# Optimization experiments

Hardware: AMD Instinct MI355X
Metric: run time of the kernel (lower is better)

## Reference

```python
import jax, jax.numpy as jnp
import numpy as np

B, T, V, F = 8, 12, 2048, 16
K_CHEB, C = 3, 64

def setup_inputs() -> dict:
    key = jax.random.key(0)
    k1, k2, k3, k4 = jax.random.split(key, 4)
    x = jax.random.normal(k1, (B, T, V, F), dtype=jnp.float32)
    Att = jax.random.uniform(k2, (B, V, V), dtype=jnp.float32)
    cheb = jax.random.normal(k3, (K_CHEB, V, V), dtype=jnp.float32) / np.sqrt(V)
    theta = jax.random.normal(k4, (K_CHEB, F, C), dtype=jnp.float32) * 0.05
    return {"x": x, "Att": Att, "cheb": cheb, "theta": theta}

def reference(x, Att, cheb, theta):
    # Attention-masked Chebyshev polynomials: S_k[b,u,v] = T_k[u,v] * Att[b,u,v]
    # (dropout from the original training-time call is omitted: eval mode)
    masked = cheb[:, None, :, :] * Att[None, :, :, :]            # (K,B,V,V)
    # rhs[b,v,f] = sum_u S_k[b,u,v] * x[b,t,u,f]  (transpose+batch_dot)
    rhs = jnp.einsum('kbuv,btuf->kbtvf', masked, x)              # (K,B,T,V,F)
    # sum over Chebyshev order k of rhs @ Theta_k, then relu
    out = jnp.einsum('kbtvf,kfc->btvc', rhs, theta)              # (B,T,V,C)
    return jax.nn.relu(out)
```

## Files before the change

### kernel.cpp

```cpp
#include <hip/hip_runtime.h>
#include <hip/hip_bf16.h>
#include <stdint.h>

#define B_  8
#define T_  12
#define V_  2048
#define F_  16
#define K_  3
#define C_  64
#define N_  192

typedef _Float16 f16;
typedef _Float16 half4v __attribute__((ext_vector_type(4)));
typedef _Float16 half8v __attribute__((ext_vector_type(8)));
typedef float    f32x4  __attribute__((ext_vector_type(4)));
typedef float    f32x16 __attribute__((ext_vector_type(16)));
typedef unsigned int u32;

__global__ __launch_bounds__(256) void prep_xt(const float* __restrict__ x,
                                               f16* __restrict__ XT) {
  int bid = blockIdx.x;
  int bt = bid >> 2, uc = bid & 3;
  int b = bt / T_, t = bt % T_;
  __shared__ float tile[64][17];
  int r  = threadIdx.x >> 2, fq = threadIdx.x & 3;
  int f  = threadIdx.x >> 4, uq = threadIdx.x & 15;
  for (int u0 = uc * 512; u0 < uc * 512 + 512; u0 += 64) {
    f32x4 v = *(const f32x4*)(x + ((size_t)(b * T_ + t) * V_ + u0 + r) * F_ + fq * 4);
    tile[r][fq * 4 + 0] = v[0];
    tile[r][fq * 4 + 1] = v[1];
    tile[r][fq * 4 + 2] = v[2];
    tile[r][fq * 4 + 3] = v[3];
    __syncthreads();
    half4v h;
    h[0] = (f16)tile[uq * 4 + 0][f];
    h[1] = (f16)tile[uq * 4 + 1][f];
    h[2] = (f16)tile[uq * 4 + 2][f];
    h[3] = (f16)tile[uq * 4 + 3][f];
    *(half4v*)(XT + (size_t)(b * N_ + t * F_ + f) * V_ + u0 + uq * 4) = h;
    __syncthreads();
  }
}

__global__ __launch_bounds__(256) void prep_chebT(const float* __restrict__ c,
                                                  f16* __restrict__ cT) {
  int bid = blockIdx.x;
  int vt = bid & 31, ut = (bid >> 5) & 31, k = bid >> 10;
  int u0 = ut * 64, v0 = vt * 64;
  __shared__ float tile[64][68];
  int tid = threadIdx.x;
  int lr = tid >> 4, lc = (tid & 15) * 4;
  const float* src = c + ((size_t)k * V_ + u0) * V_ + v0;
#pragma unroll
  for (int i = 0; i < 4; ++i) {
    f32x4 v = *(const f32x4*)(src + (size_t)(lr + 16 * i) * V_ + lc);
    tile[lr + 16 * i][lc + 0] = v[0];
    tile[lr + 16 * i][lc + 1] = v[1];
    tile[lr + 16 * i][lc + 2] = v[2];
    tile[lr + 16 * i][lc + 3] = v[3];
  }
  __syncthreads();
  int vl = tid & 63, uc0 = tid >> 6;
#pragma unroll
  for (int i = 0; i < 2; ++i) {
    int uc = uc0 + 4 * i;
    half8v h;
#pragma unroll
    for (int j = 0; j < 8; ++j) h[j] = (f16)tile[uc * 8 + j][vl];
    int vb = (v0 + vl) >> 5;
    int vi = vl & 31;
    size_t ut_idx = (size_t)(u0 >> 3) + uc;
    size_t off = ((((size_t)k * 64 + vb) * 256 + ut_idx) * 32 + vi) * 8;
    *(half8v*)(cT + off) = h;
  }
}

#define MFMA_H(a, b, c) __builtin_amdgcn_mfma_f32_32x32x16_f16(a, b, c, 0, 0, 0)

#define KS_GROUP(ks, AC, BC)                                                   \
  {                                                                            \
    const int kb = (ks) * 32 + hi * 16;                                        \
    half8v af = *(const half8v*)((AC) + vrow * 128 + (kb ^ skey));             \
    half8v b0 = *(const half8v*)((BC) + nrow0 * 128 + (kb ^ bk0));             \
    half8v b1 = *(const half8v*)((BC) + nrow1 * 128 + (kb ^ bk1));             \
    half8v b2 = *(const half8v*)((BC) + nrow2 * 128 + (kb ^ bk2));             \
    const size_t co = (size_t)(t * 8 + (ks) * 2 + hi) * 256;                   \
    half8v c0 = *(const half8v*)(chb0 + co);                                   \
    half8v c1 = *(const half8v*)(chb1 + co);                                   \
    half8v c2 = *(const half8v*)(chb2 + co);                                   \
    half8v a0 = c0 * af, a1 = c1 * af, a2 = c2 * af;                           \
    __builtin_amdgcn_s_setprio(1);                                             \
    acc[0][0] = MFMA_H(a0, b0, acc[0][0]);                                     \
    acc[0][1] = MFMA_H(a0, b1, acc[0][1]);                                     \
    acc[0][2] = MFMA_H(a0, b2, acc[0][2]);                                     \
    acc[1][0] = MFMA_H(a1, b0, acc[1][0]);                                     \
    acc[1][1] = MFMA_H(a1, b1, acc[1][1]);                                     \
    acc[1][2] = MFMA_H(a1, b2, acc[1][2]);                                     \
    acc[2][0] = MFMA_H(a2, b0, acc[2][0]);                                     \
    acc[2][1] = MFMA_H(a2, b1, acc[2][1]);                                     \
    acc[2][2] = MFMA_H(a2, b2, acc[2][2]);                                     \
    __builtin_amdgcn_s_setprio(0);                                             \
  }

template<int UH>
__global__ __launch_bounds__(256, 2) void gemm2(const float* __restrict__ Att,
                                                const f16* __restrict__ chebT,
                                                const f16* __restrict__ XT,
                                                f16* __restrict__ rhs) {
  constexpr int NSTEP = (V_ / UH) / 64;
  const int bid = blockIdx.x;
  const int vt = bid & 31;
  const int rr = bid >> 5;
  const int b  = rr / UH;
  const int uh = rr % UH;
  const int vbase = vt * 64;
  const size_t ubase = (size_t)uh * (V_ / UH);

  __shared__ char smem[65536];
  char* Bb0 = smem;
  char* Bb1 = smem + 24576;
  char* Ab0 = smem + 49152;
  char* Ab1 = smem + 57344;

  const int tid = threadIdx.x;
  const int wave = tid >> 6, lane = tid & 63;
  const int wm = wave >> 1, wn = wave & 1;
  const int hi = lane >> 5, l31 = lane & 31;
  const int vrow = wm * 32 + l31;
  const int vsub = (tid & 15) * 4, usub = (tid >> 4) * 4;

  const int skey = ((vrow + (vrow >> 3)) & 7) << 4;
  const int nrow0 = wn * 96 + l31;
  const int nrow1 = nrow0 + 32;
  const int nrow2 = nrow0 + 64;
  const int bk0 = (nrow0 & 7) << 4, bk1 = (nrow1 & 7) << 4, bk2 = (nrow2 & 7) << 4;

  const int vb = vt * 2 + wm;
  const f16* chb0 = chebT + (((size_t)vb * 256 + (ubase >> 3)) * 32 + l31) * 8;
  const f16* chb1 = chb0 + (size_t)V_ * V_;
  const f16* chb2 = chb1 + (size_t)V_ * V_;

  const float* attb = Att + (size_t)b * V_ * V_ + (ubase + usub) * V_ + vbase + vsub;
  const f16*   xtb  = XT + (size_t)b * N_ * V_ + ubase;

  f32x16 acc[3][3];
#pragma unroll
  for (int k = 0; k < 3; ++k)
#pragma unroll
    for (int nf = 0; nf < 3; ++nf) acc[k][nf] = 0;

  f32x4 pa[4];
  const int gl_c = lane & 7;

  auto stageB = [&](int t, char* Bb) {
#pragma unroll
    for (int e = 0; e < 6; ++e) {
      int slot = wave * 6 + e;
      int n = slot * 8 + (lane >> 3);
      int cc = gl_c ^ (n & 7);
      const f16* src = xtb + (size_t)n * V_ + t * 64 + cc * 8;
      __builtin_amdgcn_global_load_lds((const __attribute__((address_space(1))) u32*)src,
                                       (__attribute__((address_space(3))) u32*)(Bb + slot * 1024),
                                       16, 0, 0);
    }
  };
  auto issueAtt = [&](int t) {
#pragma unroll
    for (int i = 0; i < 4; ++i)
      pa[i] = *(const f32x4*)(attb + (size_t)(t * 64 + i) * V_);
  };
  auto writeAtt = [&](char* Aw) {
#pragma unroll
    for (int j = 0; j < 4; ++j) {
      int vr = vsub + j;
      half4v h;
      h[0] = (f16)pa[0][j]; h[1] = (f16)pa[1][j];
      h[2] = (f16)pa[2][j]; h[3] = (f16)pa[3][j];
      *(half4v*)(Aw + vr * 128 + ((usub * 2) ^ (((vr + (vr >> 3)) & 7) << 4))) = h;
    }
  };

  issueAtt(0);
  stageB(0, Bb0);
  writeAtt(Ab0);
  __syncthreads();

#pragma unroll 1
  for (int t0 = 0; t0 < NSTEP; t0 += 2) {
    {
      const int t = t0;
      issueAtt(t + 1);
      stageB(t + 1, Bb1);
      KS_GROUP(0, Ab0, Bb0)
      KS_GROUP(1, Ab0, Bb0)
      KS_GROUP(2, Ab0, Bb0)
      KS_GROUP(3, Ab0, Bb0)
      writeAtt(Ab1);
      __syncthreads();
    }
    {
      const int t = t0 + 1;
      const bool p2 = (t + 1) < NSTEP;
      if (p2) { issueAtt(t + 1); stageB(t + 1, Bb0); }
      KS_GROUP(0, Ab1, Bb1)
      KS_GROUP(1, Ab1, Bb1)
      KS_GROUP(2, Ab1, Bb1)
      KS_GROUP(3, Ab1, Bb1)
      if (p2) writeAtt(Ab0);
      __syncthreads();
    }
  }

#pragma unroll
  for (int nf = 0; nf < 3; ++nf) {
    int n = wn * 96 + nf * 32 + l31;
    int tt = n >> 4, fi = n & 15;
#pragma unroll
    for (int k = 0; k < 3; ++k) {
#pragma unroll
      for (int r = 0; r < 16; ++r) {
        int v = vbase + wm * 32 + (r & 3) + 8 * (r >> 2) + 4 * hi;
        rhs[((size_t)(b * T_ + tt) * V_ + v) * (48 * UH) + uh * 48 + k * 16 + fi] =
            (f16)acc[k][nf][r];
      }
    }
  }
}

template<int UH>
__global__ __launch_bounds__(256) void epi(const f16* __restrict__ rhs,
                                           const float* __restrict__ theta,
                                           float* __restrict__ out) {
  int wave = threadIdx.x >> 6, lane = threadIdx.x & 63;
  int row0 = blockIdx.x * 128 + wave * 32;
  int cl = lane & 31, kh = (lane >> 5) * 8;

  half8v bf[2][3];
#pragma unroll
  for (int nf = 0; nf < 2; ++nf)
#pragma unroll
    for (int ks = 0; ks < 3; ++ks) {
      half8v hb;
#pragma unroll
      for (int j = 0; j < 8; ++j)
        hb[j] = (f16)theta[(size_t)(ks * 16 + kh + j) * C_ + nf * 32 + cl];
      bf[nf][ks] = hb;
    }

  f32x16 acc0 = 0, acc1 = 0;
#pragma unroll
  for (int s = 0; s < 3 * UH; ++s) {
    half8v a = *(const half8v*)(rhs + (size_t)(row0 + cl) * (48 * UH) + s * 16 + kh);
    acc0 = __builtin_amdgcn_mfma_f32_32x32x16_f16(a, bf[0][s % 3], acc0, 0, 0, 0);
    acc1 = __builtin_amdgcn_mfma_f32_32x32x16_f16(a, bf[1][s % 3], acc1, 0, 0, 0);
  }
#pragma unroll
  for (int r = 0; r < 16; ++r) {
    int row = row0 + (r & 3) + 8 * (r >> 2) + 4 * (lane >> 5);
    out[(size_t)row * C_ + cl]      = fmaxf(acc0[r], 0.f);
    out[(size_t)row * C_ + 32 + cl] = fmaxf(acc1[r], 0.f);
  }
}

extern "C" void kernel_launch(void* const* d_in, const int* in_sizes, int n_in,
                              void* d_out, int out_size, void* d_ws, size_t ws_size,
                              hipStream_t stream) {
  const float* x     = (const float*)d_in[0];
  const float* Att   = (const float*)d_in[1];
  const float* cheb  = (const float*)d_in[2];
  const float* theta = (const float*)d_in[3];
  float* out = (float*)d_out;

  const size_t xtB   = (size_t)B_ * N_ * V_ * sizeof(f16);
  const size_t rhs2B = (size_t)B_ * T_ * V_ * 96 * sizeof(f16);
  const size_t rhs1B = rhs2B / 2;
  const size_t chB   = (size_t)K_ * V_ * V_ * sizeof(f16);

  f16* XT = (f16*)d_ws;
  prep_xt<<<B_ * T_ * 4, 256, 0, stream>>>(x, XT);

  if (ws_size >= xtB + rhs2B + chB) {
    f16* rhs = (f16*)((char*)d_ws + xtB);
    f16* cT  = (f16*)((char*)d_ws + xtB + rhs2B);
    prep_chebT<<<K_ * 32 * 32, 256, 0, stream>>>(cheb, cT);
    gemm2<2><<<B_ * 32 * 2, 256, 0, stream>>>(Att, cT, XT, rhs);
    epi<2><<<(B_ * T_ * V_) / 128, 256, 0, stream>>>(rhs, theta, out);
  } else {
    f16* rhs = (f16*)((char*)d_ws + xtB);
    f16* cT  = (f16*)((char*)d_ws + xtB + rhs1B);
    prep_chebT<<<K_ * 32 * 32, 256, 0, stream>>>(cheb, cT);
    gemm2<1><<<B_ * 32, 256, 0, stream>>>(Att, cT, XT, rhs);
    epi<1><<<(B_ * T_ * V_) / 128, 256, 0, stream>>>(rhs, theta, out);
  }
}
```

Measured before the change: 112.6 us.

## Switch main GEMM to 16x16x32 MFMA with smaller tiles and more blocks

Replaces the 32x32x16 MFMA GEMM with a 16x16x32 variant. Each block now covers 32 v-rows and half of the N=192 columns, uses half the shared memory, and runs at a higher occupancy target (4 blocks per CU). The Chebyshev transposed layout is changed to 16-row groups to match the new fragment shape. The block count quadruples to spread the work over more CUs, at the cost of re-reading Att and cheb once per N-half and running a shorter pipeline per block.

```diff
diff --git a/kernel.cpp b/kernel.cpp
--- a/kernel.cpp
+++ b/kernel.cpp
@@ -11,10 +11,10 @@
 #define N_  192
 
 typedef _Float16 f16;
+typedef _Float16 half2v __attribute__((ext_vector_type(2)));
 typedef _Float16 half4v __attribute__((ext_vector_type(4)));
 typedef _Float16 half8v __attribute__((ext_vector_type(8)));
 typedef float    f32x4  __attribute__((ext_vector_type(4)));
-typedef float    f32x16 __attribute__((ext_vector_type(16)));
 typedef unsigned int u32;
 
 __global__ __launch_bounds__(256) void prep_xt(const float* __restrict__ x,
@@ -67,95 +67,92 @@
     half8v h;
 #pragma unroll
     for (int j = 0; j < 8; ++j) h[j] = (f16)tile[uc * 8 + j][vl];
-    int vb = (v0 + vl) >> 5;
-    int vi = vl & 31;
-    size_t ut_idx = (size_t)(u0 >> 3) + uc;
-    size_t off = ((((size_t)k * 64 + vb) * 256 + ut_idx) * 32 + vi) * 8;
+    int vb16 = vt * 4 + (vl >> 4);
+    int vi   = vl & 15;
+    int ub8  = ut * 8 + uc;
+    size_t off = ((((size_t)k * 128 + vb16) * 256 + ub8) * 16 + vi) * 8;
     *(half8v*)(cT + off) = h;
   }
 }
 
-#define MFMA_H(a, b, c) __builtin_amdgcn_mfma_f32_32x32x16_f16(a, b, c, 0, 0, 0)
-
-#define KS_GROUP(ks, AC, BC)                                                   \
-  {                                                                            \
-    const int kb = (ks) * 32 + hi * 16;                                        \
-    half8v af = *(const half8v*)((AC) + vrow * 128 + (kb ^ skey));             \
-    half8v b0 = *(const half8v*)((BC) + nrow0 * 128 + (kb ^ bk0));             \
-    half8v b1 = *(const half8v*)((BC) + nrow1 * 128 + (kb ^ bk1));             \
-    half8v b2 = *(const half8v*)((BC) + nrow2 * 128 + (kb ^ bk2));             \
-    const size_t co = (size_t)(t * 8 + (ks) * 2 + hi) * 256;                   \
-    half8v c0 = *(const half8v*)(chb0 + co);                                   \
-    half8v c1 = *(const half8v*)(chb1 + co);                                   \
-    half8v c2 = *(const half8v*)(chb2 + co);                                   \
-    half8v a0 = c0 * af, a1 = c1 * af, a2 = c2 * af;                           \
-    __builtin_amdgcn_s_setprio(1);                                             \
-    acc[0][0] = MFMA_H(a0, b0, acc[0][0]);                                     \
-    acc[0][1] = MFMA_H(a0, b1, acc[0][1]);                                     \
-    acc[0][2] = MFMA_H(a0, b2, acc[0][2]);                                     \
-    acc[1][0] = MFMA_H(a1, b0, acc[1][0]);                                     \
-    acc[1][1] = MFMA_H(a1, b1, acc[1][1]);                                     \
-    acc[1][2] = MFMA_H(a1, b2, acc[1][2]);                                     \
-    acc[2][0] = MFMA_H(a2, b0, acc[2][0]);                                     \
-    acc[2][1] = MFMA_H(a2, b1, acc[2][1]);                                     \
-    acc[2][2] = MFMA_H(a2, b2, acc[2][2]);                                     \
-    __builtin_amdgcn_s_setprio(0);                                             \
+#define MFMA16(a, b, c) __builtin_amdgcn_mfma_f32_16x16x32_f16(a, b, c, 0, 0, 0)
+
+#define KS_STEP(ks, AC, BC, tt)                                                 \
+  {                                                                             \
+    const int kb = (ks) * 64 + lg * 16;                                         \
+    half8v b0 = *(const half8v*)((BC) + n0 * 128 + (kb ^ bk0));                 \
+    half8v b1 = *(const half8v*)((BC) + n1 * 128 + (kb ^ bk1));                 \
+    half8v b2 = *(const half8v*)((BC) + n2 * 128 + (kb ^ bk2));                 \
+    half8v af = *(const half8v*)((AC) + vr * 128 + (kb ^ ak));                  \
+    const size_t co = (size_t)((tt) * 8 + (ks) * 4) * 128;                      \
+    _Pragma("unroll")                                                           \
+    for (int k = 0; k < 3; ++k) {                                               \
+      half8v cf = *(const half8v*)(chb[k] + co);                                \
+      half8v a = cf * af;                                                       \
+      __builtin_amdgcn_s_setprio(1);                                            \
+      acc[k][0] = MFMA16(a, b0, acc[k][0]);                                     \
+      acc[k][1] = MFMA16(a, b1, acc[k][1]);                                     \
+      acc[k][2] = MFMA16(a, b2, acc[k][2]);                                     \
+      __builtin_amdgcn_s_setprio(0);                                            \
+    }                                                                           \
   }
 
 template<int UH>
-__global__ __launch_bounds__(256, 2) void gemm2(const float* __restrict__ Att,
+__global__ __launch_bounds__(256, 4) void gemm3(const float* __restrict__ Att,
                                                 const f16* __restrict__ chebT,
                                                 const f16* __restrict__ XT,
                                                 f16* __restrict__ rhs) {
   constexpr int NSTEP = (V_ / UH) / 64;
   const int bid = blockIdx.x;
-  const int vt = bid & 31;
-  const int rr = bid >> 5;
-  const int b  = rr / UH;
-  const int uh = rr % UH;
-  const int vbase = vt * 64;
+  const int vt = (bid & 7) | (((bid >> 3) & 7) << 3);
+  const int r2 = bid >> 6;
+  const int nh = r2 & 1;
+  const int r3 = r2 >> 1;
+  const int uh = r3 % UH;
+  const int b  = r3 / UH;
+  const int vbase = vt * 32;
   const size_t ubase = (size_t)uh * (V_ / UH);
 
-  __shared__ char smem[65536];
+  __shared__ char smem[32768];
   char* Bb0 = smem;
-  char* Bb1 = smem + 24576;
-  char* Ab0 = smem + 49152;
-  char* Ab1 = smem + 57344;
+  char* Bb1 = smem + 12288;
+  char* Ab0 = smem + 24576;
+  char* Ab1 = smem + 28672;
 
   const int tid = threadIdx.x;
   const int wave = tid >> 6, lane = tid & 63;
-  const int wm = wave >> 1, wn = wave & 1;
-  const int hi = lane >> 5, l31 = lane & 31;
-  const int vrow = wm * 32 + l31;
-  const int vsub = (tid & 15) * 4, usub = (tid >> 4) * 4;
-
-  const int skey = ((vrow + (vrow >> 3)) & 7) << 4;
-  const int nrow0 = wn * 96 + l31;
-  const int nrow1 = nrow0 + 32;
-  const int nrow2 = nrow0 + 64;
-  const int bk0 = (nrow0 & 7) << 4, bk1 = (nrow1 & 7) << 4, bk2 = (nrow2 & 7) << 4;
-
-  const int vb = vt * 2 + wm;
-  const f16* chb0 = chebT + (((size_t)vb * 256 + (ubase >> 3)) * 32 + l31) * 8;
-  const f16* chb1 = chb0 + (size_t)V_ * V_;
-  const f16* chb2 = chb1 + (size_t)V_ * V_;
-
+  const int wv = wave >> 1, wn = wave & 1;
+  const int l15 = lane & 15, lg = lane >> 4;
+
+  const int vr = wv * 16 + l15;
+  const int ak = (vr & 7) << 4;
+  const int n0 = wn * 48 + l15, n1 = n0 + 16, n2 = n0 + 32;
+  const int bk0 = (n0 & 7) << 4, bk1 = (n1 & 7) << 4, bk2 = (n2 & 7) << 4;
+
+  const int vb16 = vt * 2 + wv;
+  const f16* chb[3];
+#pragma unroll
+  for (int k = 0; k < 3; ++k)
+    chb[k] = chebT + ((((size_t)k * 128 + vb16) * 256 + (ubase >> 3)) * 16) * 8
+           + lg * 128 + l15 * 8;
+
+  const int vsub = (tid & 7) * 4;
+  const int usub = (tid >> 3) * 2;
   const float* attb = Att + (size_t)b * V_ * V_ + (ubase + usub) * V_ + vbase + vsub;
-  const f16*   xtb  = XT + (size_t)b * N_ * V_ + ubase;
-
-  f32x16 acc[3][3];
+
+  const f16* xtb = XT + (size_t)b * N_ * V_ + (size_t)(nh * 96) * V_ + ubase;
+  const int gl_c = lane & 7;
+
+  f32x4 acc[3][3];
 #pragma unroll
   for (int k = 0; k < 3; ++k)
 #pragma unroll
-    for (int nf = 0; nf < 3; ++nf) acc[k][nf] = 0;
-
-  f32x4 pa[4];
-  const int gl_c = lane & 7;
+    for (int ni = 0; ni < 3; ++ni) acc[k][ni] = 0;
 
   auto stageB = [&](int t, char* Bb) {
 #pragma unroll
-    for (int e = 0; e < 6; ++e) {
-      int slot = wave * 6 + e;
+    for (int e = 0; e < 3; ++e) {
+      int slot = wave * 3 + e;
       int n = slot * 8 + (lane >> 3);
       int cc = gl_c ^ (n & 7);
       const f16* src = xtb + (size_t)n * V_ + t * 64 + cc * 8;
@@ -164,64 +161,57 @@
                                        16, 0, 0);
     }
   };
-  auto issueAtt = [&](int t) {
-#pragma unroll
-    for (int i = 0; i < 4; ++i)
-      pa[i] = *(const f32x4*)(attb + (size_t)(t * 64 + i) * V_);
+  auto writeAtt = [&](const f32x4& p0, const f32x4& p1, char* Aw) {
+#pragma unroll
+    for (int j = 0; j < 4; ++j) {
+      int v2 = vsub + j;
+      half2v h;
+      h[0] = (f16)p0[j]; h[1] = (f16)p1[j];
+      *(half2v*)(Aw + v2 * 128 + ((usub * 2) ^ ((v2 & 7) << 4))) = h;
+    }
   };
-  auto writeAtt = [&](char* Aw) {
-#pragma unroll
-    for (int j = 0; j < 4; ++j) {
-      int vr = vsub + j;
-      half4v h;
-      h[0] = (f16)pa[0][j]; h[1] = (f16)pa[1][j];
-      h[2] = (f16)pa[2][j]; h[3] = (f16)pa[3][j];
-      *(half4v*)(Aw + vr * 128 + ((usub * 2) ^ (((vr + (vr >> 3)) & 7) << 4))) = h;
-    }
-  };
-
-  issueAtt(0);
-  stageB(0, Bb0);
-  writeAtt(Ab0);
+
+  {
+    f32x4 p0 = *(const f32x4*)(attb);
+    f32x4 p1 = *(const f32x4*)(attb + V_);
+    stageB(0, Bb0);
+    writeAtt(p0, p1, Ab0);
+  }
   __syncthreads();
 
 #pragma unroll 1
-  for (int t0 = 0; t0 < NSTEP; t0 += 2) {
-    {
-      const int t = t0;
-      issueAtt(t + 1);
-      stageB(t + 1, Bb1);
-      KS_GROUP(0, Ab0, Bb0)
-      KS_GROUP(1, Ab0, Bb0)
-      KS_GROUP(2, Ab0, Bb0)
-      KS_GROUP(3, Ab0, Bb0)
-      writeAtt(Ab1);
-      __syncthreads();
-    }
-    {
-      const int t = t0 + 1;
-      const bool p2 = (t + 1) < NSTEP;
-      if (p2) { issueAtt(t + 1); stageB(t + 1, Bb0); }
-      KS_GROUP(0, Ab1, Bb1)
-      KS_GROUP(1, Ab1, Bb1)
-      KS_GROUP(2, Ab1, Bb1)
-      KS_GROUP(3, Ab1, Bb1)
-      if (p2) writeAtt(Ab0);
-      __syncthreads();
-    }
-  }
-
-#pragma unroll
-  for (int nf = 0; nf < 3; ++nf) {
-    int n = wn * 96 + nf * 32 + l31;
+  for (int t = 0; t < NSTEP; ++t) {
+    char* Bc = (t & 1) ? Bb1 : Bb0;
+    char* Bn = (t & 1) ? Bb0 : Bb1;
+    char* Ac = (t & 1) ? Ab1 : Ab0;
+    char* An = (t & 1) ? Ab0 : Ab1;
+    const bool pref = (t + 1) < NSTEP;
+
+    f32x4 p0, p1;
+    if (pref) {
+      p0 = *(const f32x4*)(attb + (size_t)((t + 1) * 64) * V_);
+      p1 = *(const f32x4*)(attb + (size_t)((t + 1) * 64 + 1) * V_);
+      stageB(t + 1, Bn);
+    }
+
+    KS_STEP(0, Ac, Bc, t)
+    KS_STEP(1, Ac, Bc, t)
+
+    if (pref) writeAtt(p0, p1, An);
+    __syncthreads();
+  }
+
+#pragma unroll
+  for (int ni = 0; ni < 3; ++ni) {
+    int n = nh * 96 + wn * 48 + ni * 16 + l15;
     int tt = n >> 4, fi = n & 15;
 #pragma unroll
     for (int k = 0; k < 3; ++k) {
 #pragma unroll
-      for (int r = 0; r < 16; ++r) {
-        int v = vbase + wm * 32 + (r & 3) + 8 * (r >> 2) + 4 * hi;
+      for (int r = 0; r < 4; ++r) {
+        int v = vbase + wv * 16 + lg * 4 + r;
         rhs[((size_t)(b * T_ + tt) * V_ + v) * (48 * UH) + uh * 48 + k * 16 + fi] =
-            (f16)acc[k][nf][r];
+            (f16)acc[k][ni][r];
       }
     }
   }
@@ -247,6 +237,7 @@
       bf[nf][ks] = hb;
     }
 
+  typedef float f32x16 __attribute__((ext_vector_type(16)));
   f32x16 acc0 = 0, acc1 = 0;
 #pragma unroll
   for (int s = 0; s < 3 * UH; ++s) {
@@ -283,13 +274,13 @@
     f16* rhs = (f16*)((char*)d_ws + xtB);
     f16* cT  = (f16*)((char*)d_ws + xtB + rhs2B);
     prep_chebT<<<K_ * 32 * 32, 256, 0, stream>>>(cheb, cT);
-    gemm2<2><<<B_ * 32 * 2, 256, 0, stream>>>(Att, cT, XT, rhs);
+    gemm3<2><<<B_ * 64 * 2 * 2, 256, 0, stream>>>(Att, cT, XT, rhs);
     epi<2><<<(B_ * T_ * V_) / 128, 256, 0, stream>>>(rhs, theta, out);
   } else {
     f16* rhs = (f16*)((char*)d_ws + xtB);
     f16* cT  = (f16*)((char*)d_ws + xtB + rhs1B);
     prep_chebT<<<K_ * 32 * 32, 256, 0, stream>>>(cheb, cT);
-    gemm2<1><<<B_ * 32, 256, 0, stream>>>(Att, cT, XT, rhs);
+    gemm3<1><<<B_ * 64 * 2 * 1, 256, 0, stream>>>(Att, cT, XT, rhs);
     epi<1><<<(B_ * T_ * V_) / 128, 256, 0, stream>>>(rhs, theta, out);
   }
 }
```

Result: slower. 153.8 us (+36.6%).
